# Performance work log

Hardware: AMD Instinct MI355X
Metric: run time of the kernel (lower is better)

The kernel has to match this reference:

```python
import jax, jax.numpy as jnp
import numpy as np

N_NODES = 100000
N_EDGES = 3200000
F_IN = 256
HID = 64
N_CLS = 16


def setup_inputs() -> dict:
    key = jax.random.key(0)
    ks = jax.random.split(key, 12)
    x = jax.random.normal(ks[0], (N_NODES, F_IN), dtype=jnp.float32)
    edge_index = jax.random.randint(ks[1], (2, N_EDGES), 0, N_NODES, dtype=jnp.int32)
    w_mul = jax.random.normal(ks[2], (N_EDGES, 1), dtype=jnp.float32)
    s1 = 1.0 / np.sqrt(F_IN)
    s2 = 1.0 / np.sqrt(HID)
    # layer 1 params
    lin1_w = jax.random.uniform(ks[3], (HID, F_IN), minval=-s1, maxval=s1, dtype=jnp.float32)
    lin1_b = jax.random.uniform(ks[4], (HID,), minval=-s1, maxval=s1, dtype=jnp.float32)
    mlp1_w0 = jax.random.uniform(ks[5], (HID, 1), minval=-1.0, maxval=1.0, dtype=jnp.float32)
    mlp1_w1 = jax.random.uniform(ks[6], (HID, HID), minval=-s2, maxval=s2, dtype=jnp.float32)
    mlp1_b1 = jax.random.uniform(ks[7], (HID,), minval=-s2, maxval=s2, dtype=jnp.float32)
    # layer 2 params
    lin2_w = jax.random.uniform(ks[8], (N_CLS, HID), minval=-s2, maxval=s2, dtype=jnp.float32)
    lin2_b = jax.random.uniform(ks[9], (N_CLS,), minval=-s2, maxval=s2, dtype=jnp.float32)
    mlp2_w0 = jax.random.uniform(ks[10], (HID, 1), minval=-1.0, maxval=1.0, dtype=jnp.float32)
    mlp2_w1 = jax.random.uniform(ks[11], (N_CLS, HID), minval=-s2, maxval=s2, dtype=jnp.float32)
    mlp2_b1 = jnp.zeros((N_CLS,), dtype=jnp.float32)
    return dict(x=x, edge_index=edge_index, w_mul=w_mul,
                lin1_w=lin1_w, lin1_b=lin1_b, mlp1_w0=mlp1_w0, mlp1_w1=mlp1_w1, mlp1_b1=mlp1_b1,
                lin2_w=lin2_w, lin2_b=lin2_b, mlp2_w0=mlp2_w0, mlp2_w1=mlp2_w1, mlp2_b1=mlp2_b1)


def curv_layer(x, src, dst, w_mul, lin_w, lin_b, m_w0, m_w1, m_b1, n_nodes):
    # dense projection: [N, out]
    h = x @ lin_w.T + lin_b
    # per-edge weight MLP: Linear(1,HID,no bias) -> LeakyReLU(0.2) -> Linear(HID,out,bias)
    ew = jax.nn.leaky_relu(w_mul @ m_w0.T, negative_slope=0.2) @ m_w1.T + m_b1  # [E, out]
    # segment softmax keyed by source node (PyG softmax(out_weight, edge_index[0]))
    emax = jax.ops.segment_max(ew, src, num_segments=n_nodes)  # [N, out]
    e = jnp.exp(ew - emax[src])
    esum = jax.ops.segment_sum(e, src, num_segments=n_nodes)
    alpha = e / (esum[src] + 1e-16)  # [E, out]
    # message = alpha * x_j (x_j = h[src]); scatter-add at destination
    msg = alpha * h[src]
    return jax.ops.segment_sum(msg, dst, num_segments=n_nodes)  # [N, out]


def reference(x, edge_index, w_mul,
              lin1_w, lin1_b, mlp1_w0, mlp1_w1, mlp1_b1,
              lin2_w, lin2_b, mlp2_w0, mlp2_w1, mlp2_b1):
    src, dst = edge_index[0], edge_index[1]
    n = x.shape[0]
    # eval mode: dropout(p=0.8) is identity
    h = curv_layer(x, src, dst, w_mul, lin1_w, lin1_b, mlp1_w0, mlp1_w1, mlp1_b1, n)
    h = jax.nn.elu(h)
    h = curv_layer(h, src, dst, w_mul, lin2_w, lin2_b, mlp2_w0, mlp2_w1, mlp2_b1, n)
    return jax.nn.log_softmax(h, axis=1)
```

## Files before the change

### kernel.cpp

```cpp
#include <hip/hip_runtime.h>
#include <math.h>

#define FIN 256
#define HID 64
#define NCLS 16
#define BSH 8
#define BWD (1 << BSH)
#define NBKMAX 512
#define CAP 9216
#define CHUNK_S 16384
#define CHUNK_D 8192

__global__ __launch_bounds__(512) void init_kernel(int* gcur_s, int* gcur_d) {
    int tid = threadIdx.x;
    gcur_s[tid] = tid * CAP;
    gcur_d[tid] = tid * CAP;
}

__global__ __launch_bounds__(512) void stage_kernel(const int* __restrict__ ei,
                                                    const float* __restrict__ w,
                                                    int* gcur_s, int* gcur_d,
                                                    unsigned int* st_s, uint2* st_d,
                                                    int E, int nchunk_s) {
    __shared__ int lh[NBKMAX];
    __shared__ int lofs[NBKMAX];
    __shared__ int lcur[NBKMAX];
    __shared__ int gbase[NBKMAX];
    __shared__ uint2 buf2[CHUNK_D];
    unsigned int* buf1 = (unsigned int*)buf2;
    int tid = threadIdx.x;
    int side = (blockIdx.x >= nchunk_s) ? 1 : 0;
    lh[tid] = 0;
    __syncthreads();
    if (!side) {
        int base = blockIdx.x * CHUNK_S;
        #pragma unroll
        for (int j = 0; j < CHUNK_S / 512; j++) {
            int e = base + tid + j * 512;
            if (e < E) atomicAdd(&lh[((unsigned)ei[e]) >> BSH], 1);
        }
    } else {
        int base = (blockIdx.x - nchunk_s) * CHUNK_D;
        #pragma unroll
        for (int j = 0; j < CHUNK_D / 512; j++) {
            int e = base + tid + j * 512;
            if (e < E) atomicAdd(&lh[((unsigned)ei[E + e]) >> BSH], 1);
        }
    }
    __syncthreads();
    int v = lh[tid];
    lofs[tid] = v;
    __syncthreads();
    for (int off = 1; off < 512; off <<= 1) {
        int add = (tid >= off) ? lofs[tid - off] : 0;
        __syncthreads();
        lofs[tid] += add;
        __syncthreads();
    }
    int ex = lofs[tid] - v;
    lofs[tid] = ex;
    lcur[tid] = ex;
    __syncthreads();
    if (!side) {
        int base = blockIdx.x * CHUNK_S;
        #pragma unroll
        for (int j = 0; j < CHUNK_S / 512; j++) {
            int e = base + tid + j * 512;
            if (e < E) {
                int s = ei[e];
                unsigned int rec = (__float_as_uint(w[e]) & 0xFFFFFF00u) | (unsigned int)(s & 0xFF);
                int p = atomicAdd(&lcur[((unsigned)s) >> BSH], 1);
                buf1[p] = rec;
            }
        }
    } else {
        int base = (blockIdx.x - nchunk_s) * CHUNK_D;
        #pragma unroll
        for (int j = 0; j < CHUNK_D / 512; j++) {
            int e = base + tid + j * 512;
            if (e < E) {
                int d = ei[E + e];
                int s = ei[e];
                unsigned int rec = (__float_as_uint(w[e]) & 0xFFFFFF00u) | (unsigned int)(d & 0xFF);
                int p = atomicAdd(&lcur[((unsigned)d) >> BSH], 1);
                buf2[p] = make_uint2((unsigned int)s, rec);
            }
        }
    }
    __syncthreads();
    {
        int c = lh[tid];
        if (c) gbase[tid] = atomicAdd(side ? &gcur_d[tid] : &gcur_s[tid], c);
    }
    __syncthreads();
    int wv = tid >> 6, lane = tid & 63;
    if (!side) {
        for (int b = wv; b < NBKMAX; b += 8) {
            int c = lh[b];
            int ls = lofs[b], gs = gbase[b];
            for (int i = lane; i < c; i += 64) st_s[gs + i] = buf1[ls + i];
        }
    } else {
        for (int b = wv; b < NBKMAX; b += 8) {
            int c = lh[b];
            int ls = lofs[b], gs = gbase[b];
            for (int i = lane; i < c; i += 64) st_d[gs + i] = buf2[ls + i];
        }
    }
}

__global__ __launch_bounds__(512) void bucket_scan_kernel(const int* gcur_s, const int* gcur_d,
                                                          int* bbase_s, int* bbase_d,
                                                          int* offs_s, int* offs_d,
                                                          int N, int nbk, int E) {
    int side = blockIdx.x;
    const int* gc = side ? gcur_d : gcur_s;
    int* bb = side ? bbase_d : bbase_s;
    __shared__ int tmp[512];
    int tid = threadIdx.x;
    int v = (tid < nbk) ? (gc[tid] - tid * CAP) : 0;
    tmp[tid] = v;
    __syncthreads();
    for (int off = 1; off < 512; off <<= 1) {
        int add = (tid >= off) ? tmp[tid - off] : 0;
        __syncthreads();
        tmp[tid] += add;
        __syncthreads();
    }
    if (tid < nbk) bb[tid] = tmp[tid] - v;
    if (tid == 0) {
        bb[nbk] = E;
        (side ? offs_d : offs_s)[N] = E;
    }
}

__global__ __launch_bounds__(256) void bucket_build_s_kernel(const int* __restrict__ bbase,
                                                             const unsigned int* __restrict__ st,
                                                             int* offs, float* t_s, int N) {
    int b = blockIdx.x;
    int r0 = bbase[b];
    int cnt = bbase[b + 1] - r0;
    if (cnt > CAP) cnt = CAP;
    size_t sb = (size_t)b * CAP;
    int n0 = b << BSH;
    int nn = min(BWD, N - n0);
    __shared__ int lh[BWD];
    __shared__ int lofs[BWD];
    __shared__ float buf[CAP];
    int tid = threadIdx.x;
    lh[tid] = 0;
    __syncthreads();
    for (int i = tid; i < cnt; i += 256) atomicAdd(&lh[st[sb + i] & 0xFFu], 1);
    __syncthreads();
    int v = lh[tid];
    lofs[tid] = v;
    __syncthreads();
    for (int off = 1; off < 256; off <<= 1) {
        int add = (tid >= off) ? lofs[tid - off] : 0;
        __syncthreads();
        lofs[tid] += add;
        __syncthreads();
    }
    int ex = lofs[tid] - v;
    if (tid < nn) offs[n0 + tid] = r0 + ex;
    lofs[tid] = ex;
    __syncthreads();
    for (int i = tid; i < cnt; i += 256) {
        unsigned int rec = st[sb + i];
        int p = atomicAdd(&lofs[rec & 0xFFu], 1);
        buf[p] = __uint_as_float(rec & 0xFFFFFF00u);
    }
    __syncthreads();
    for (int i = tid; i < cnt; i += 256) t_s[r0 + i] = buf[i];
}

__global__ __launch_bounds__(256) void bucket_build_d_kernel(const int* __restrict__ bbase,
                                                             const uint2* __restrict__ st,
                                                             int* offs, int2* ed, int N) {
    int b = blockIdx.x;
    int r0 = bbase[b];
    int cnt = bbase[b + 1] - r0;
    if (cnt > CAP) cnt = CAP;
    size_t sb = (size_t)b * CAP;
    int n0 = b << BSH;
    int nn = min(BWD, N - n0);
    __shared__ int lh[BWD];
    __shared__ int lofs[BWD];
    __shared__ int2 buf[CAP];
    int tid = threadIdx.x;
    lh[tid] = 0;
    __syncthreads();
    for (int i = tid; i < cnt; i += 256) atomicAdd(&lh[st[sb + i].y & 0xFFu], 1);
    __syncthreads();
    int v = lh[tid];
    lofs[tid] = v;
    __syncthreads();
    for (int off = 1; off < 256; off <<= 1) {
        int add = (tid >= off) ? lofs[tid - off] : 0;
        __syncthreads();
        lofs[tid] += add;
        __syncthreads();
    }
    int ex = lofs[tid] - v;
    if (tid < nn) offs[n0 + tid] = r0 + ex;
    lofs[tid] = ex;
    __syncthreads();
    for (int i = tid; i < cnt; i += 256) {
        uint2 rec = st[sb + i];
        int p = atomicAdd(&lofs[rec.y & 0xFFu], 1);
        buf[p] = make_int2((int)rec.x, (int)(rec.y & 0xFFFFFF00u));
    }
    __syncthreads();
    for (int i = tid; i < cnt; i += 256) ed[r0 + i] = buf[i];
}

#define LOG2E 1.44269504088896340736f
__global__ void prep_kernel(const float* __restrict__ w0a, const float* __restrict__ w1a,
                            const float* __restrict__ w0b, const float* __restrict__ w1b,
                            float* Ap1, float* An1, float* Ap2, float* An2) {
    int tid = threadIdx.x;
    if (tid < 64) {
        float ap = 0.f, an = 0.f;
        for (int j = 0; j < 64; j++) {
            float w0 = w0a[j];
            float w1 = w1a[tid * 64 + j];
            ap += w0 * ((w0 >= 0.f) ? 1.f : 0.2f) * w1;
            an += w0 * ((w0 <= 0.f) ? 1.f : 0.2f) * w1;
        }
        Ap1[tid] = ap * LOG2E; An1[tid] = an * LOG2E;
    } else if (tid < 80) {
        int k = tid - 64;
        float ap = 0.f, an = 0.f;
        for (int j = 0; j < 64; j++) {
            float w0 = w0b[j];
            float w1 = w1b[k * 64 + j];
            ap += w0 * ((w0 >= 0.f) ? 1.f : 0.2f) * w1;
            an += w0 * ((w0 <= 0.f) ? 1.f : 0.2f) * w1;
        }
        Ap2[k] = ap * LOG2E; An2[k] = an * LOG2E;
    }
}

__global__ __launch_bounds__(256) void esum1_kernel(const int* __restrict__ offs,
                                                    const float* __restrict__ t_s,
                                                    const float* __restrict__ Ap,
                                                    const float* __restrict__ An,
                                                    float* __restrict__ inv, int N) {
    int node = blockIdx.x * 4 + (threadIdx.x >> 6);
    int k = threadIdx.x & 63;
    if (node >= N) return;
    int s0 = offs[node], s1 = offs[node + 1];
    float ap = Ap[k], an = An[k];
    float sum = 0.f;
    int i = s0;
    for (; i + 3 < s1; i += 4) {
        float t0 = t_s[i], t1 = t_s[i + 1], t2 = t_s[i + 2], t3 = t_s[i + 3];
        sum += __builtin_amdgcn_exp2f(t0 * ((t0 >= 0.f) ? ap : an));
        sum += __builtin_amdgcn_exp2f(t1 * ((t1 >= 0.f) ? ap : an));
        sum += __builtin_amdgcn_exp2f(t2 * ((t2 >= 0.f) ? ap : an));
        sum += __builtin_amdgcn_exp2f(t3 * ((t3 >= 0.f) ? ap : an));
    }
    for (; i < s1; i++) {
        float t = t_s[i];
        sum += __builtin_amdgcn_exp2f(t * ((t >= 0.f) ? ap : an));
    }
    inv[(size_t)node * 64 + k] = (s1 > s0) ? 1.f / (sum + 1e-16f) : 0.f;
}

__global__ __launch_bounds__(256) void esum2_kernel(const int* __restrict__ offs,
                                                    const float* __restrict__ t_s,
                                                    const float* __restrict__ Ap,
                                                    const float* __restrict__ An,
                                                    float* __restrict__ inv, int N) {
    int node = blockIdx.x * 16 + (threadIdx.x >> 4);
    int k = threadIdx.x & 15;
    if (node >= N) return;
    int s0 = offs[node], s1 = offs[node + 1];
    float ap = Ap[k], an = An[k];
    float sum = 0.f;
    int i = s0;
    for (; i + 3 < s1; i += 4) {
        float t0 = t_s[i], t1 = t_s[i + 1], t2 = t_s[i + 2], t3 = t_s[i + 3];
        sum += __builtin_amdgcn_exp2f(t0 * ((t0 >= 0.f) ? ap : an));
        sum += __builtin_amdgcn_exp2f(t1 * ((t1 >= 0.f) ? ap : an));
        sum += __builtin_amdgcn_exp2f(t2 * ((t2 >= 0.f) ? ap : an));
        sum += __builtin_amdgcn_exp2f(t3 * ((t3 >= 0.f) ? ap : an));
    }
    for (; i < s1; i++) {
        float t = t_s[i];
        sum += __builtin_amdgcn_exp2f(t * ((t >= 0.f) ? ap : an));
    }
    inv[(size_t)node * 16 + k] = (s1 > s0) ? 1.f / (sum + 1e-16f) : 0.f;
}

__device__ __forceinline__ unsigned int bf16rn(float f) {
    unsigned int u = __float_as_uint(f);
    return (u + 0x7fffu + ((u >> 16) & 1u)) >> 16;
}

#define GP 68
__global__ __launch_bounds__(256) void gemm1_kernel(const float* __restrict__ x,
                                                    const float* __restrict__ W,
                                                    const float* __restrict__ b,
                                                    const float* __restrict__ inv,
                                                    uint2* __restrict__ g1, int N) {
    __shared__ float xs[32][GP];
    __shared__ float wsh[32][GP];
    int block_row = blockIdx.x * 64;
    int tid = threadIdx.x;
    int tr = tid / 16, tc = tid % 16;
    float acc[4][4] = {{0.f}};
    for (int k0 = 0; k0 < FIN; k0 += 32) {
        #pragma unroll
        for (int i = 0; i < 2; i++) {
            int idx = tid + i * 256;
            int r = idx >> 3;
            int c4 = idx & 7;
            int gr = block_row + r;
            float4 v = (gr < N) ? *(const float4*)&x[(size_t)gr * FIN + k0 + c4 * 4]
                                : make_float4(0.f, 0.f, 0.f, 0.f);
            xs[c4 * 4 + 0][r] = v.x; xs[c4 * 4 + 1][r] = v.y;
            xs[c4 * 4 + 2][r] = v.z; xs[c4 * 4 + 3][r] = v.w;
            float4 wv = *(const float4*)&W[r * FIN + k0 + c4 * 4];
            wsh[c4 * 4 + 0][r] = wv.x; wsh[c4 * 4 + 1][r] = wv.y;
            wsh[c4 * 4 + 2][r] = wv.z; wsh[c4 * 4 + 3][r] = wv.w;
        }
        __syncthreads();
        #pragma unroll
        for (int kk = 0; kk < 32; kk++) {
            float4 xv = *(const float4*)&xs[kk][tr * 4];
            float4 wv = *(const float4*)&wsh[kk][tc * 4];
            acc[0][0] += xv.x * wv.x; acc[0][1] += xv.x * wv.y; acc[0][2] += xv.x * wv.z; acc[0][3] += xv.x * wv.w;
            acc[1][0] += xv.y * wv.x; acc[1][1] += xv.y * wv.y; acc[1][2] += xv.y * wv.z; acc[1][3] += xv.y * wv.w;
            acc[2][0] += xv.z * wv.x; acc[2][1] += xv.z * wv.y; acc[2][2] += xv.z * wv.z; acc[2][3] += xv.z * wv.w;
            acc[3][0] += xv.w * wv.x; acc[3][1] += xv.w * wv.y; acc[3][2] += xv.w * wv.z; acc[3][3] += xv.w * wv.w;
        }
        __syncthreads();
    }
    float4 bv = ((const float4*)b)[tc];
    #pragma unroll
    for (int i = 0; i < 4; i++) {
        int gr = block_row + tr * 4 + i;
        if (gr < N) {
            float4 iv = *(const float4*)&inv[(size_t)gr * 64 + tc * 4];
            float o0 = (acc[i][0] + bv.x) * iv.x;
            float o1 = (acc[i][1] + bv.y) * iv.y;
            float o2 = (acc[i][2] + bv.z) * iv.z;
            float o3 = (acc[i][3] + bv.w) * iv.w;
            uint2 p;
            p.x = bf16rn(o0) | (bf16rn(o1) << 16);
            p.y = bf16rn(o2) | (bf16rn(o3) << 16);
            g1[(size_t)gr * 16 + tc] = p;
        }
    }
}

__global__ __launch_bounds__(256) void gemm2_kernel(const float* __restrict__ x2,
                                                    const float* __restrict__ W2,
                                                    const float* __restrict__ b2,
                                                    const float* __restrict__ inv,
                                                    float* __restrict__ g2, int N) {
    __shared__ float ws[16][GP];
    __shared__ float xs[16][GP];
    __shared__ float bs[16];
    int tid = threadIdx.x;
    {
        int c = tid >> 4, j4 = tid & 15;
        float4 v = ((const float4*)W2)[tid];
        ws[c][j4 * 4 + 0] = v.x; ws[c][j4 * 4 + 1] = v.y;
        ws[c][j4 * 4 + 2] = v.z; ws[c][j4 * 4 + 3] = v.w;
    }
    if (tid < 16) bs[tid] = b2[tid];
    int node0 = blockIdx.x * 16;
    {
        int r = tid >> 4, c4 = tid & 15;
        int gn = node0 + r;
        float4 v = (gn < N) ? *(const float4*)&x2[(size_t)gn * 64 + c4 * 4]
                            : make_float4(0.f, 0.f, 0.f, 0.f);
        xs[r][c4 * 4 + 0] = v.x; xs[r][c4 * 4 + 1] = v.y;
        xs[r][c4 * 4 + 2] = v.z; xs[r][c4 * 4 + 3] = v.w;
    }
    __syncthreads();
    int node_l = tid >> 4, col = tid & 15;
    int gn = node0 + node_l;
    if (gn >= N) return;
    float acc = bs[col];
    #pragma unroll
    for (int j4 = 0; j4 < 16; j4++) {
        float4 xv = *(const float4*)&xs[node_l][j4 * 4];
        float4 wv = *(const float4*)&ws[col][j4 * 4];
        acc += xv.x * wv.x + xv.y * wv.y + xv.z * wv.z + xv.w * wv.w;
    }
    g2[(size_t)gn * NCLS + col] = acc * inv[(size_t)gn * NCLS + col];
}

__global__ __launch_bounds__(256) void agg1_kernel(const int* __restrict__ offs,
                                                   const int2* __restrict__ ed,
                                                   const float* __restrict__ Ap,
                                                   const float* __restrict__ An,
                                                   const uint4* __restrict__ g,
                                                   float* __restrict__ x2, int N) {
    int node = blockIdx.x * 32 + (threadIdx.x >> 3);
    int l = threadIdx.x & 7;
    if (node >= N) return;
    int d0 = offs[node], d1 = offs[node + 1];
    float4 ap0 = ((const float4*)Ap)[l * 2], ap1 = ((const float4*)Ap)[l * 2 + 1];
    float4 an0 = ((const float4*)An)[l * 2], an1 = ((const float4*)An)[l * 2 + 1];
    float4 acc0 = make_float4(0.f, 0.f, 0.f, 0.f);
    float4 acc1 = make_float4(0.f, 0.f, 0.f, 0.f);
    int i = d0;
    int end4 = d0 + ((d1 - d0) & ~3);
    for (; i < end4; i += 4) {
        int2 e[4];
        #pragma unroll
        for (int j = 0; j < 4; j++) e[j] = ed[i + j];
        uint4 gv[4];
        #pragma unroll
        for (int j = 0; j < 4; j++)
            gv[j] = g[((size_t)e[j].x << 3) + l];
        #pragma unroll
        for (int j = 0; j < 4; j++) {
            float t = __int_as_float(e[j].y);
            float4 a0 = (t >= 0.f) ? ap0 : an0;
            float4 a1 = (t >= 0.f) ? ap1 : an1;
            acc0.x += __builtin_amdgcn_exp2f(t * a0.x) * __uint_as_float(gv[j].x << 16);
            acc0.y += __builtin_amdgcn_exp2f(t * a0.y) * __uint_as_float(gv[j].x & 0xffff0000u);
            acc0.z += __builtin_amdgcn_exp2f(t * a0.z) * __uint_as_float(gv[j].y << 16);
            acc0.w += __builtin_amdgcn_exp2f(t * a0.w) * __uint_as_float(gv[j].y & 0xffff0000u);
            acc1.x += __builtin_amdgcn_exp2f(t * a1.x) * __uint_as_float(gv[j].z << 16);
            acc1.y += __builtin_amdgcn_exp2f(t * a1.y) * __uint_as_float(gv[j].z & 0xffff0000u);
            acc1.z += __builtin_amdgcn_exp2f(t * a1.z) * __uint_as_float(gv[j].w << 16);
            acc1.w += __builtin_amdgcn_exp2f(t * a1.w) * __uint_as_float(gv[j].w & 0xffff0000u);
        }
    }
    for (; i < d1; i++) {
        int2 e = ed[i];
        float t = __int_as_float(e.y);
        float4 a0 = (t >= 0.f) ? ap0 : an0;
        float4 a1 = (t >= 0.f) ? ap1 : an1;
        uint4 gv = g[((size_t)e.x << 3) + l];
        acc0.x += __builtin_amdgcn_exp2f(t * a0.x) * __uint_as_float(gv.x << 16);
        acc0.y += __builtin_amdgcn_exp2f(t * a0.y) * __uint_as_float(gv.x & 0xffff0000u);
        acc0.z += __builtin_amdgcn_exp2f(t * a0.z) * __uint_as_float(gv.y << 16);
        acc0.w += __builtin_amdgcn_exp2f(t * a0.w) * __uint_as_float(gv.y & 0xffff0000u);
        acc1.x += __builtin_amdgcn_exp2f(t * a1.x) * __uint_as_float(gv.z << 16);
        acc1.y += __builtin_amdgcn_exp2f(t * a1.y) * __uint_as_float(gv.z & 0xffff0000u);
        acc1.z += __builtin_amdgcn_exp2f(t * a1.z) * __uint_as_float(gv.w << 16);
        acc1.w += __builtin_amdgcn_exp2f(t * a1.w) * __uint_as_float(gv.w & 0xffff0000u);
    }
    float4 o0, o1;
    o0.x = (acc0.x > 0.f) ? acc0.x : (__expf(acc0.x) - 1.f);
    o0.y = (acc0.y > 0.f) ? acc0.y : (__expf(acc0.y) - 1.f);
    o0.z = (acc0.z > 0.f) ? acc0.z : (__expf(acc0.z) - 1.f);
    o0.w = (acc0.w > 0.f) ? acc0.w : (__expf(acc0.w) - 1.f);
    o1.x = (acc1.x > 0.f) ? acc1.x : (__expf(acc1.x) - 1.f);
    o1.y = (acc1.y > 0.f) ? acc1.y : (__expf(acc1.y) - 1.f);
    o1.z = (acc1.z > 0.f) ? acc1.z : (__expf(acc1.z) - 1.f);
    o1.w = (acc1.w > 0.f) ? acc1.w : (__expf(acc1.w) - 1.f);
    float* dst = x2 + ((size_t)node << 6) + l * 8;
    *(float4*)(dst) = o0;
    *(float4*)(dst + 4) = o1;
}

__global__ __launch_bounds__(256) void agg2_kernel(const int* __restrict__ offs,
                                                   const int2* __restrict__ ed,
                                                   const float* __restrict__ Ap,
                                                   const float* __restrict__ An,
                                                   const float* __restrict__ g,
                                                   float* __restrict__ out, int N) {
    int node = blockIdx.x * 64 + (threadIdx.x >> 2);
    int l = threadIdx.x & 3;
    if (node >= N) return;
    int d0 = offs[node], d1 = offs[node + 1];
    float4 ap = ((const float4*)Ap)[l];
    float4 an = ((const float4*)An)[l];
    float4 acc = make_float4(0.f, 0.f, 0.f, 0.f);
    int i = d0;
    int end8 = d0 + ((d1 - d0) & ~7);
    for (; i < end8; i += 8) {
        int2 e[8];
        #pragma unroll
        for (int j = 0; j < 8; j++) e[j] = ed[i + j];
        float4 gv[8];
        #pragma unroll
        for (int j = 0; j < 8; j++)
            gv[j] = *(const float4*)(g + ((size_t)e[j].x << 4) + l * 4);
        #pragma unroll
        for (int j = 0; j < 8; j++) {
            float t = __int_as_float(e[j].y);
            float4 a = (t >= 0.f) ? ap : an;
            acc.x += __builtin_amdgcn_exp2f(t * a.x) * gv[j].x;
            acc.y += __builtin_amdgcn_exp2f(t * a.y) * gv[j].y;
            acc.z += __builtin_amdgcn_exp2f(t * a.z) * gv[j].z;
            acc.w += __builtin_amdgcn_exp2f(t * a.w) * gv[j].w;
        }
    }
    for (; i < d1; i++) {
        int2 e = ed[i];
        float t = __int_as_float(e.y);
        float4 a = (t >= 0.f) ? ap : an;
        float4 gv = *(const float4*)(g + ((size_t)e.x << 4) + l * 4);
        acc.x += __builtin_amdgcn_exp2f(t * a.x) * gv.x;
        acc.y += __builtin_amdgcn_exp2f(t * a.y) * gv.y;
        acc.z += __builtin_amdgcn_exp2f(t * a.z) * gv.z;
        acc.w += __builtin_amdgcn_exp2f(t * a.w) * gv.w;
    }
    float m = fmaxf(fmaxf(acc.x, acc.y), fmaxf(acc.z, acc.w));
    m = fmaxf(m, __shfl_xor(m, 1, 4));
    m = fmaxf(m, __shfl_xor(m, 2, 4));
    float s = __expf(acc.x - m) + __expf(acc.y - m) + __expf(acc.z - m) + __expf(acc.w - m);
    s += __shfl_xor(s, 1, 4);
    s += __shfl_xor(s, 2, 4);
    float lse = m + __logf(s);
    float4 o = make_float4(acc.x - lse, acc.y - lse, acc.z - lse, acc.w - lse);
    *(float4*)(out + ((size_t)node << 4) + l * 4) = o;
}

extern "C" void kernel_launch(void* const* d_in, const int* in_sizes, int n_in,
                              void* d_out, int out_size, void* d_ws, size_t ws_size,
                              hipStream_t stream) {
    const float* x      = (const float*)d_in[0];
    const int*   ei     = (const int*)d_in[1];
    const float* wmul   = (const float*)d_in[2];
    const float* lin1_w = (const float*)d_in[3];
    const float* lin1_b = (const float*)d_in[4];
    const float* m1w0   = (const float*)d_in[5];
    const float* m1w1   = (const float*)d_in[6];
    const float* lin2_w = (const float*)d_in[8];
    const float* lin2_b = (const float*)d_in[9];
    const float* m2w0   = (const float*)d_in[10];
    const float* m2w1   = (const float*)d_in[11];

    int N = in_sizes[0] / FIN;
    int E = in_sizes[1] / 2;
    int nbk = (N + BWD - 1) >> BSH;
    int nchunk_s = (E + CHUNK_S - 1) / CHUNK_S;
    int nchunk_d = (E + CHUNK_D - 1) / CHUNK_D;

    char* ws = (char*)d_ws;
    auto alloc = [&](size_t bytes) {
        char* p = ws;
        ws += (bytes + 255) & ~(size_t)255;
        return p;
    };
    int*   gcur_s  = (int*)alloc(NBKMAX * 4);
    int*   gcur_d  = (int*)alloc(NBKMAX * 4);
    int*   bbase_s = (int*)alloc((NBKMAX + 1) * 4);
    int*   bbase_d = (int*)alloc((NBKMAX + 1) * 4);
    float* Ap1     = (float*)alloc(64 * 4);
    float* An1     = (float*)alloc(64 * 4);
    float* Ap2     = (float*)alloc(16 * 4);
    float* An2     = (float*)alloc(16 * 4);
    int*   offs_s  = (int*)alloc((size_t)(N + 1) * 4);
    int*   offs_d  = (int*)alloc((size_t)(N + 1) * 4);
    float* t_s     = (float*)alloc((size_t)E * 4);
    int2*  ed      = (int2*)alloc((size_t)E * 8);
    char*  reg = ws;
    unsigned int* st_s = (unsigned int*)(reg);
    uint2*        st_d = (uint2*)(reg + (((size_t)nbk * CAP * 4 + 255) & ~(size_t)255));
    float* inv1 = (float*)(reg);
    float* x2   = (float*)(reg);
    char*  regB = reg + (((size_t)N * 64 * 4 + 255) & ~(size_t)255);
    uint2* g1   = (uint2*)(regB);
    float* inv2 = (float*)(regB + ((size_t)N * 16 * 8));
    float* g2   = (float*)(regB + ((size_t)N * 16 * 8) + ((size_t)N * 16 * 4));

    init_kernel<<<1, 512, 0, stream>>>(gcur_s, gcur_d);
    prep_kernel<<<1, 128, 0, stream>>>(m1w0, m1w1, m2w0, m2w1, Ap1, An1, Ap2, An2);
    stage_kernel<<<nchunk_s + nchunk_d, 512, 0, stream>>>(ei, wmul, gcur_s, gcur_d,
                                                          st_s, st_d, E, nchunk_s);
    bucket_scan_kernel<<<2, 512, 0, stream>>>(gcur_s, gcur_d, bbase_s, bbase_d,
                                              offs_s, offs_d, N, nbk, E);
    bucket_build_s_kernel<<<nbk, 256, 0, stream>>>(bbase_s, st_s, offs_s, t_s, N);
    bucket_build_d_kernel<<<nbk, 256, 0, stream>>>(bbase_d, st_d, offs_d, ed, N);
    esum1_kernel<<<(N + 3) / 4, 256, 0, stream>>>(offs_s, t_s, Ap1, An1, inv1, N);
    gemm1_kernel<<<(N + 63) / 64, 256, 0, stream>>>(x, lin1_w, lin1_b, inv1, g1, N);
    agg1_kernel<<<(N + 31) / 32, 256, 0, stream>>>(offs_d, ed, Ap1, An1, (const uint4*)g1, x2, N);
    esum2_kernel<<<(N + 15) / 16, 256, 0, stream>>>(offs_s, t_s, Ap2, An2, inv2, N);
    gemm2_kernel<<<(N + 15) / 16, 256, 0, stream>>>(x2, lin2_w, lin2_b, inv2, g2, N);
    agg2_kernel<<<(N + 63) / 64, 256, 0, stream>>>(offs_d, ed, Ap2, An2, g2, (float*)d_out, N);
}
```

Before: 518.1 us.

## Use split-bf16 MFMA for first-layer projection GEMM

The first-layer dense projection (x @ W1^T), previously an FP32 FMA GEMM, now runs on bf16 MFMA matrix instructions. Each fp32 operand is split into a high and a residual low bf16 part and three MFMAs are accumulated to keep roughly fp32 accuracy. Tiles are stored in XOR-swizzled shared memory to avoid bank conflicts, and the next K chunk is prefetched into registers while the current one is computed. The cost is extra conversion work and more shared memory, plus a small accuracy loss from dropping the low×low term.

```diff
diff --git a/kernel.cpp b/kernel.cpp
--- a/kernel.cpp
+++ b/kernel.cpp
@@ -10,6 +10,9 @@
 #define CAP 9216
 #define CHUNK_S 16384
 #define CHUNK_D 8192
+
+typedef __attribute__((ext_vector_type(8))) short bf16x8;
+typedef __attribute__((ext_vector_type(4))) float f32x4;
 
 __global__ __launch_bounds__(512) void init_kernel(int* gcur_s, int* gcur_d) {
     int tid = threadIdx.x;
@@ -298,63 +301,124 @@
     return (u + 0x7fffu + ((u >> 16) & 1u)) >> 16;
 }
 
-#define GP 68
-__global__ __launch_bounds__(256) void gemm1_kernel(const float* __restrict__ x,
-                                                    const float* __restrict__ W,
-                                                    const float* __restrict__ b,
-                                                    const float* __restrict__ inv,
-                                                    uint2* __restrict__ g1, int N) {
-    __shared__ float xs[32][GP];
-    __shared__ float wsh[32][GP];
+__device__ __forceinline__ void cvt8_split(const float4 a, const float4 b, bf16x8& h, bf16x8& l) {
+    float f[8] = {a.x, a.y, a.z, a.w, b.x, b.y, b.z, b.w};
+    #pragma unroll
+    for (int j = 0; j < 8; j++) {
+        unsigned int uh = bf16rn(f[j]);
+        float hf = __uint_as_float(uh << 16);
+        float r = f[j] - hf;
+        unsigned int ul = bf16rn(r);
+        h[j] = (short)uh;
+        l[j] = (short)ul;
+    }
+}
+
+#define KCH 64
+__global__ __launch_bounds__(256, 4) void gemm1_kernel(const float* __restrict__ x,
+                                                       const float* __restrict__ W,
+                                                       const float* __restrict__ b,
+                                                       const float* __restrict__ inv,
+                                                       uint2* __restrict__ g1, int N) {
+    __shared__ unsigned short xh[64 * KCH];
+    __shared__ unsigned short xl[64 * KCH];
+    __shared__ unsigned short wh[64 * KCH];
+    __shared__ unsigned short wl[64 * KCH];
+    int tid = threadIdx.x;
     int block_row = blockIdx.x * 64;
-    int tid = threadIdx.x;
-    int tr = tid / 16, tc = tid % 16;
-    float acc[4][4] = {{0.f}};
-    for (int k0 = 0; k0 < FIN; k0 += 32) {
-        #pragma unroll
-        for (int i = 0; i < 2; i++) {
-            int idx = tid + i * 256;
-            int r = idx >> 3;
-            int c4 = idx & 7;
-            int gr = block_row + r;
-            float4 v = (gr < N) ? *(const float4*)&x[(size_t)gr * FIN + k0 + c4 * 4]
-                                : make_float4(0.f, 0.f, 0.f, 0.f);
-            xs[c4 * 4 + 0][r] = v.x; xs[c4 * 4 + 1][r] = v.y;
-            xs[c4 * 4 + 2][r] = v.z; xs[c4 * 4 + 3][r] = v.w;
-            float4 wv = *(const float4*)&W[r * FIN + k0 + c4 * 4];
-            wsh[c4 * 4 + 0][r] = wv.x; wsh[c4 * 4 + 1][r] = wv.y;
-            wsh[c4 * 4 + 2][r] = wv.z; wsh[c4 * 4 + 3][r] = wv.w;
-        }
-        __syncthreads();
-        #pragma unroll
-        for (int kk = 0; kk < 32; kk++) {
-            float4 xv = *(const float4*)&xs[kk][tr * 4];
-            float4 wv = *(const float4*)&wsh[kk][tc * 4];
-            acc[0][0] += xv.x * wv.x; acc[0][1] += xv.x * wv.y; acc[0][2] += xv.x * wv.z; acc[0][3] += xv.x * wv.w;
-            acc[1][0] += xv.y * wv.x; acc[1][1] += xv.y * wv.y; acc[1][2] += xv.y * wv.z; acc[1][3] += xv.y * wv.w;
-            acc[2][0] += xv.z * wv.x; acc[2][1] += xv.z * wv.y; acc[2][2] += xv.z * wv.z; acc[2][3] += xv.z * wv.w;
-            acc[3][0] += xv.w * wv.x; acc[3][1] += xv.w * wv.y; acc[3][2] += xv.w * wv.z; acc[3][3] += xv.w * wv.w;
-        }
-        __syncthreads();
-    }
-    float4 bv = ((const float4*)b)[tc];
+    float4 pf[4][2];
+    auto load_chunk = [&](int kbase) {
+        #pragma unroll
+        for (int i = 0; i < 4; i++) {
+            int t = tid + i * 256;
+            if (t < 512) {
+                int r = t >> 3, g = t & 7;
+                int gr = block_row + r;
+                if (gr < N) {
+                    const float* p = &x[(size_t)gr * FIN + kbase + g * 8];
+                    pf[i][0] = *(const float4*)p;
+                    pf[i][1] = *(const float4*)(p + 4);
+                } else {
+                    pf[i][0] = make_float4(0.f, 0.f, 0.f, 0.f);
+                    pf[i][1] = make_float4(0.f, 0.f, 0.f, 0.f);
+                }
+            } else {
+                int r = (t - 512) >> 3, g = t & 7;
+                const float* p = &W[r * FIN + kbase + g * 8];
+                pf[i][0] = *(const float4*)p;
+                pf[i][1] = *(const float4*)(p + 4);
+            }
+        }
+    };
+    auto write_chunk = [&]() {
+        #pragma unroll
+        for (int i = 0; i < 4; i++) {
+            int t = tid + i * 256;
+            int r = (t & 511) >> 3, g = t & 7;
+            int gs = g ^ (r & 7);
+            bf16x8 h, l;
+            cvt8_split(pf[i][0], pf[i][1], h, l);
+            if (t < 512) {
+                *(bf16x8*)&xh[r * KCH + gs * 8] = h;
+                *(bf16x8*)&xl[r * KCH + gs * 8] = l;
+            } else {
+                *(bf16x8*)&wh[r * KCH + gs * 8] = h;
+                *(bf16x8*)&wl[r * KCH + gs * 8] = l;
+            }
+        }
+    };
+
+    int wv = tid >> 6, l = tid & 63;
+    int lrow = l & 15, kg = l >> 4;
+    f32x4 acc[4];
     #pragma unroll
-    for (int i = 0; i < 4; i++) {
-        int gr = block_row + tr * 4 + i;
-        if (gr < N) {
-            float4 iv = *(const float4*)&inv[(size_t)gr * 64 + tc * 4];
-            float o0 = (acc[i][0] + bv.x) * iv.x;
-            float o1 = (acc[i][1] + bv.y) * iv.y;
-            float o2 = (acc[i][2] + bv.z) * iv.z;
-            float o3 = (acc[i][3] + bv.w) * iv.w;
+    for (int c = 0; c < 4; c++) acc[c] = (f32x4){0.f, 0.f, 0.f, 0.f};
+
+    const unsigned short* xrow_h = &xh[(wv * 16 + lrow) * KCH];
+    const unsigned short* xrow_l = &xl[(wv * 16 + lrow) * KCH];
+
+    load_chunk(0);
+    for (int kc = 0; kc < FIN / KCH; kc++) {
+        write_chunk();
+        __syncthreads();
+        if (kc + 1 < FIN / KCH) load_chunk((kc + 1) * KCH);
+        #pragma unroll
+        for (int s = 0; s < 2; s++) {
+            int gB = ((s * 4 + kg) ^ (lrow & 7)) * 8;
+            bf16x8 bh = *(const bf16x8*)&xrow_h[gB];
+            bf16x8 bl = *(const bf16x8*)&xrow_l[gB];
+            #pragma unroll
+            for (int c = 0; c < 4; c++) {
+                int wro = (c * 16 + lrow) * KCH + gB;
+                bf16x8 ah = *(const bf16x8*)&wh[wro];
+                bf16x8 al = *(const bf16x8*)&wl[wro];
+                acc[c] = __builtin_amdgcn_mfma_f32_16x16x32_bf16(ah, bh, acc[c], 0, 0, 0);
+                acc[c] = __builtin_amdgcn_mfma_f32_16x16x32_bf16(ah, bl, acc[c], 0, 0, 0);
+                acc[c] = __builtin_amdgcn_mfma_f32_16x16x32_bf16(al, bh, acc[c], 0, 0, 0);
+            }
+        }
+        __syncthreads();
+    }
+    int node = block_row + wv * 16 + lrow;
+    if (node < N) {
+        #pragma unroll
+        for (int c = 0; c < 4; c++) {
+            int colb = c * 16 + kg * 4;
+            float4 bv = *(const float4*)&b[colb];
+            float4 iv = *(const float4*)&inv[(size_t)node * 64 + colb];
+            float o0 = (acc[c].x + bv.x) * iv.x;
+            float o1 = (acc[c].y + bv.y) * iv.y;
+            float o2 = (acc[c].z + bv.z) * iv.z;
+            float o3 = (acc[c].w + bv.w) * iv.w;
             uint2 p;
             p.x = bf16rn(o0) | (bf16rn(o1) << 16);
             p.y = bf16rn(o2) | (bf16rn(o3) << 16);
-            g1[(size_t)gr * 16 + tc] = p;
-        }
-    }
-}
-
+            g1[(size_t)node * 16 + (colb >> 2)] = p;
+        }
+    }
+}
+
+#define GP 68
 __global__ __launch_bounds__(256) void gemm2_kernel(const float* __restrict__ x2,
                                                     const float* __restrict__ W2,
                                                     const float* __restrict__ b2,
```

New measurement: 500.0 us. -3.5%, faster.
